# Kernel optimization log

Measured on AMD Instinct MI355X. Metric: run time of the kernel, lower is better.

The kernel has to match this reference:

```python
import jax, jax.numpy as jnp
import numpy as np
import math

IN_DIM = 2048
OUT_DIM = 2048
BATCH = 4096
BN_EPS = 1e-5


def setup_inputs() -> dict:
    key = jax.random.key(0)
    ks = jax.random.split(key, 6)
    x = jax.random.normal(ks[0], (BATCH, IN_DIM), dtype=jnp.float32)
    # scale ~ N(1.0, 0.1), translate = 0
    scale = 1.0 + 0.1 * jax.random.normal(ks[1], (1, IN_DIM), dtype=jnp.float32)
    translate = jnp.zeros((1, IN_DIM), dtype=jnp.float32)
    # kaiming-normal-ish init for wave_weight (fan_in), orthogonal-ish for base_weight
    wave_weight = jax.random.normal(ks[2], (OUT_DIM, IN_DIM), dtype=jnp.float32) * np.sqrt(2.0 / IN_DIM)
    bw = jax.random.normal(ks[3], (OUT_DIM, IN_DIM), dtype=jnp.float32)
    q, _ = jnp.linalg.qr(bw.T)  # (IN_DIM, OUT_DIM) orthonormal columns
    base_weight = q.T.astype(jnp.float32)
    gamma = jnp.ones((OUT_DIM,), dtype=jnp.float32)
    beta = jnp.zeros((OUT_DIM,), dtype=jnp.float32)
    return {"x": x, "scale": scale, "translate": translate,
            "wave_weight": wave_weight, "base_weight": base_weight,
            "gamma": gamma, "beta": beta}


def reference(x, scale, translate, wave_weight, base_weight, gamma, beta):
    # Bio wavelet: pi^-1/4 * cos(3u) * exp(-0.5 u^2), u = (x - t) / clamp(s, 1e-3)
    u = (x - translate) / jnp.maximum(scale, 1e-3)            # (B, in)
    wavelet = (math.pi ** -0.25) * jnp.cos(3.0 * u) * jnp.exp(-0.5 * u * u)
    # einsum 'boi,oi->bo' with singleton o broadcast == plain matmul
    wave_out = jnp.einsum('bi,oi->bo', wavelet, wave_weight)  # (B, out)
    base_out = jnp.einsum('bi,oi->bo', x, base_weight)        # (B, out)
    y = wave_out + 0.3 * base_out
    # BatchNorm1d (training mode: batch statistics, biased variance)
    mean = jnp.mean(y, axis=0)
    var = jnp.mean(jnp.square(y - mean), axis=0)
    out = gamma * (y - mean) * jax.lax.rsqrt(var + BN_EPS) + beta
    # dropout treated as identity (deterministic reference)
    return out
```

## Files before the change

kernel.cpp:

```cpp
#include <hip/hip_runtime.h>
#include <stdint.h>

#define IN_DIM 2048
#define OUT_DIM 2048
#define BATCH 4096
#define KDIM (2 * IN_DIM)
#define KROWB (KDIM * 2)
#define KH 2048
#define NTT 32
#define BN_EPS 1e-5f

typedef __attribute__((ext_vector_type(8))) short bf16x8;
typedef __attribute__((ext_vector_type(4))) float f32x4;

__device__ __forceinline__ unsigned short f2bf(float f) {
  union { float f; unsigned u; } v; v.f = f;
  unsigned r = v.u + 0x7FFFu + ((v.u >> 16) & 1u);
  return (unsigned short)(r >> 16);
}

__global__ void prep_act(const float* __restrict__ x,
                         const float* __restrict__ scale,
                         const float* __restrict__ translate,
                         unsigned short* __restrict__ A) {
  int e = (blockIdx.x * 256 + threadIdx.x) * 4;
  int b = e / IN_DIM;
  int i = e % IN_DIM;
  float4 xv = *(const float4*)(x + e);
  float4 sv = *(const float4*)(scale + i);
  float4 tv = *(const float4*)(translate + i);
  const float c = 0.7511255444649425f;
  float u0 = (xv.x - tv.x) / fmaxf(sv.x, 1e-3f);
  float u1 = (xv.y - tv.y) / fmaxf(sv.y, 1e-3f);
  float u2 = (xv.z - tv.z) / fmaxf(sv.z, 1e-3f);
  float u3 = (xv.w - tv.w) / fmaxf(sv.w, 1e-3f);
  ushort4 wv, xb;
  wv.x = f2bf(c * __cosf(3.0f * u0) * __expf(-0.5f * u0 * u0));
  wv.y = f2bf(c * __cosf(3.0f * u1) * __expf(-0.5f * u1 * u1));
  wv.z = f2bf(c * __cosf(3.0f * u2) * __expf(-0.5f * u2 * u2));
  wv.w = f2bf(c * __cosf(3.0f * u3) * __expf(-0.5f * u3 * u3));
  xb.x = f2bf(xv.x); xb.y = f2bf(xv.y); xb.z = f2bf(xv.z); xb.w = f2bf(xv.w);
  *(ushort4*)(A + (size_t)b * KDIM + i) = wv;
  *(ushort4*)(A + (size_t)b * KDIM + IN_DIM + i) = xb;
}

__global__ void prep_w(const float* __restrict__ ww,
                       const float* __restrict__ bw,
                       unsigned short* __restrict__ W) {
  int e = (blockIdx.x * 256 + threadIdx.x) * 4;
  int o = e / IN_DIM;
  int k = e % IN_DIM;
  float4 a = *(const float4*)(ww + e);
  float4 b = *(const float4*)(bw + e);
  ushort4 wa, wb;
  wa.x = f2bf(a.x); wa.y = f2bf(a.y); wa.z = f2bf(a.z); wa.w = f2bf(a.w);
  wb.x = f2bf(0.3f * b.x); wb.y = f2bf(0.3f * b.y);
  wb.z = f2bf(0.3f * b.z); wb.w = f2bf(0.3f * b.w);
  *(ushort4*)(W + (size_t)o * KDIM + k) = wa;
  *(ushort4*)(W + (size_t)o * KDIM + IN_DIM + k) = wb;
}


#define GLDS(gp, lo) __builtin_amdgcn_global_load_lds( \
    (const __attribute__((address_space(1))) void*)(gp), \
    (__attribute__((address_space(3))) void*)(lds + (lo) + ldsl), 16, 0, 0)

#define STG(u_, gp_, t_) do { \
  GLDS((gp_) + (size_t)(t_) * 128, (u_)); \
  GLDS((gp_) + (size_t)64 * KROWB + (size_t)(t_) * 128, (u_) + 8192); \
} while (0)

#define LDA4(mh, ss) do { \
  af[0] = *(const bf16x8*)(lds + P + rA + ((mh) * 4 + 0) * 2048 + (ss)); \
  af[1] = *(const bf16x8*)(lds + P + rA + ((mh) * 4 + 1) * 2048 + (ss)); \
  af[2] = *(const bf16x8*)(lds + P + rA + ((mh) * 4 + 2) * 2048 + (ss)); \
  af[3] = *(const bf16x8*)(lds + P + rA + ((mh) * 4 + 3) * 2048 + (ss)); \
} while (0)

#define LDB4(dst, ss) do { \
  dst[0] = *(const bf16x8*)(lds + P + rB + 0 * 2048 + (ss)); \
  dst[1] = *(const bf16x8*)(lds + P + rB + 1 * 2048 + (ss)); \
  dst[2] = *(const bf16x8*)(lds + P + rB + 2 * 2048 + (ss)); \
  dst[3] = *(const bf16x8*)(lds + P + rB + 3 * 2048 + (ss)); \
} while (0)

#define MM16(mh, bfr) do { \
  __builtin_amdgcn_s_setprio(1); \
  _Pragma("unroll") for (int i2 = 0; i2 < 4; ++i2) \
  _Pragma("unroll") for (int j2 = 0; j2 < 4; ++j2) \
    acc[(mh) * 4 + i2][j2] = __builtin_amdgcn_mfma_f32_16x16x32_bf16( \
        af[i2], bfr[j2], acc[(mh) * 4 + i2][j2], 0, 0, 0); \
  __builtin_amdgcn_s_setprio(0); \
} while (0)

#define LGKM0() asm volatile("s_waitcnt lgkmcnt(0)" ::: "memory")
#define VMW0()  asm volatile("s_waitcnt vmcnt(0)" ::: "memory")
#define BAR()   do { asm volatile("" ::: "memory"); __builtin_amdgcn_s_barrier(); \
                     asm volatile("" ::: "memory"); } while (0)

#define KTILE(u, DOST) do { \
  const int P = ((u) & 1) << 16; \
  const int Q = P ^ 65536; \
  LDA4(0, s0); LDB4(b0, s0); \
  if (DOST) { STG(Q + 32768, bS0, (u) + 1); STG(Q + 49152, bS1, (u) + 1); \
              STG(Q + 0, aS0, (u) + 1); STG(Q + 16384, aS1, (u) + 1); } \
  BAR(); MM16(0, b0); LGKM0(); BAR(); \
  LDA4(1, s0); \
  BAR(); MM16(1, b0); LGKM0(); BAR(); \
  LDA4(0, s1); LDB4(b1, s1); \
  BAR(); MM16(0, b1); LGKM0(); BAR(); \
  LDA4(1, s1); \
  BAR(); MM16(1, b1); LGKM0(); if (DOST) VMW0(); BAR(); \
} while (0)

__global__ __launch_bounds__(512, 2) void gemm256(
    const unsigned short* __restrict__ A,
    const unsigned short* __restrict__ W,
    float* __restrict__ P0, float* __restrict__ P1) {
  __shared__ char lds[131072];
  const int tid = threadIdx.x;
  const int lane = tid & 63;
  const int wave = tid >> 6;
  const int wm = wave >> 2;
  const int wn = wave & 3;

  const int sw = ((blockIdx.x & 7) << 5) | (blockIdx.x >> 3);
  const int kz = sw >> 7;
  const int brow = ((sw >> 3) & 15) * 256;
  const int bcol = (sw & 7) * 256;
  const size_t kb = (size_t)kz * (KH * 2);

  const int srow = tid >> 3;
  const int gc16 = (tid & 7) ^ (srow & 7);
  const char* aS0 = (const char*)A + (size_t)(brow + srow) * KROWB + kb + gc16 * 16;
  const char* aS1 = aS0 + (size_t)128 * KROWB;
  const char* bS0 = (const char*)W + (size_t)(bcol + srow) * KROWB + kb + gc16 * 16;
  const char* bS1 = bS0 + (size_t)128 * KROWB;
  const int ldsl = wave * 1024;

  const int rA = (wm * 128 + (lane & 15)) * 128;
  const int rB = 32768 + (wn * 64 + (lane & 15)) * 128;
  const int s0 = (((lane >> 4)    ) ^ (lane & 7)) << 4;
  const int s1 = ((4 + (lane >> 4)) ^ (lane & 7)) << 4;

  f32x4 acc[8][4];
#pragma unroll
  for (int m = 0; m < 8; ++m)
#pragma unroll
    for (int n = 0; n < 4; ++n)
      acc[m][n] = (f32x4){0.f, 0.f, 0.f, 0.f};
  bf16x8 af[4], b0[4], b1[4];

  STG(32768, bS0, 0); STG(49152, bS1, 0); STG(0, aS0, 0); STG(16384, aS1, 0);
  VMW0(); BAR();

  for (int u = 0; u < NTT - 1; ++u)
    KTILE(u, 1);
  KTILE(NTT - 1, 0);

  float* Pz = kz ? P1 : P0;
  const int r0 = brow + wm * 128 + (lane >> 4) * 4;
  const int c0 = bcol + wn * 64 + (lane & 15);
#pragma unroll
  for (int m = 0; m < 8; ++m)
#pragma unroll
    for (int n = 0; n < 4; ++n)
#pragma unroll
      for (int j = 0; j < 4; ++j)
        Pz[(size_t)(r0 + m * 16 + j) * OUT_DIM + (c0 + n * 16)] = acc[m][n][j];
}

__global__ void colstats2(const float* __restrict__ P0,
                          const float* __restrict__ P1,
                          float* __restrict__ sums, float* __restrict__ sqs) {
  int col = (blockIdx.x & 7) * 256 + threadIdx.x;
  int r0 = (blockIdx.x >> 3) * 128;
  float s = 0.f, q = 0.f;
  for (int r = 0; r < 128; ++r) {
    size_t idx = (size_t)(r0 + r) * OUT_DIM + col;
    float v = P0[idx] + P1[idx];
    s += v;
    q += v * v;
  }
  atomicAdd(&sums[col], s);
  atomicAdd(&sqs[col], q);
}

__global__ void bnorm2(const float* __restrict__ P1, float* __restrict__ Y,
                       const float* __restrict__ sums, const float* __restrict__ sqs,
                       const float* __restrict__ gamma, const float* __restrict__ beta) {
  int e = (blockIdx.x * 256 + threadIdx.x) * 4;
  int c = e % OUT_DIM;
  float4 y = *(float4*)(Y + e);
  float4 p = *(const float4*)(P1 + e);
  y.x += p.x; y.y += p.y; y.z += p.z; y.w += p.w;
  float4 s = *(const float4*)(sums + c);
  float4 q = *(const float4*)(sqs + c);
  float4 g = *(const float4*)(gamma + c);
  float4 bb = *(const float4*)(beta + c);
  const float invB = 1.0f / (float)BATCH;
  float m0 = s.x * invB, m1 = s.y * invB, m2 = s.z * invB, m3 = s.w * invB;
  float i0 = rsqrtf(q.x * invB - m0 * m0 + BN_EPS);
  float i1 = rsqrtf(q.y * invB - m1 * m1 + BN_EPS);
  float i2 = rsqrtf(q.z * invB - m2 * m2 + BN_EPS);
  float i3 = rsqrtf(q.w * invB - m3 * m3 + BN_EPS);
  y.x = g.x * (y.x - m0) * i0 + bb.x;
  y.y = g.y * (y.y - m1) * i1 + bb.y;
  y.z = g.z * (y.z - m2) * i2 + bb.z;
  y.w = g.w * (y.w - m3) * i3 + bb.w;
  *(float4*)(Y + e) = y;
}

extern "C" void kernel_launch(void* const* d_in, const int* in_sizes, int n_in,
                              void* d_out, int out_size, void* d_ws, size_t ws_size,
                              hipStream_t stream) {
  const float* x         = (const float*)d_in[0];
  const float* scale     = (const float*)d_in[1];
  const float* translate = (const float*)d_in[2];
  const float* ww        = (const float*)d_in[3];
  const float* bw        = (const float*)d_in[4];
  const float* gamma     = (const float*)d_in[5];
  const float* beta      = (const float*)d_in[6];
  float* out = (float*)d_out;

  char* ws = (char*)d_ws;
  unsigned short* A = (unsigned short*)ws;
  unsigned short* W = (unsigned short*)(ws + 33554432);
  float* P1   = (float*)(ws + 50331648);
  float* sums = (float*)(ws + 83886080);
  float* sqs  = sums + OUT_DIM;

  hipMemsetAsync(sums, 0, 2 * OUT_DIM * sizeof(float), stream);
  prep_act<<<(BATCH * IN_DIM) / 1024, 256, 0, stream>>>(x, scale, translate, A);
  prep_w<<<(OUT_DIM * IN_DIM) / 1024, 256, 0, stream>>>(ww, bw, W);
  gemm256<<<256, 512, 0, stream>>>(A, W, out, P1);
  colstats2<<<256, 256, 0, stream>>>(out, P1, sums, sqs);
  bnorm2<<<(BATCH * OUT_DIM) / 1024, 256, 0, stream>>>(P1, out, sums, sqs, gamma, beta);
}
```

Measured before the change: 125.3 us.

## Switch GEMM to four-stage LDS ring with 32-wide K tiles

```diff
diff --git a/kernel.cpp b/kernel.cpp
--- a/kernel.cpp
+++ b/kernel.cpp
@@ -7,7 +7,7 @@
 #define KDIM (2 * IN_DIM)
 #define KROWB (KDIM * 2)
 #define KH 2048
-#define NTT 32
+#define NTT 64
 #define BN_EPS 1e-5f
 
 typedef __attribute__((ext_vector_type(8))) short bf16x8;
@@ -65,25 +65,6 @@
     (const __attribute__((address_space(1))) void*)(gp), \
     (__attribute__((address_space(3))) void*)(lds + (lo) + ldsl), 16, 0, 0)
 
-#define STG(u_, gp_, t_) do { \
-  GLDS((gp_) + (size_t)(t_) * 128, (u_)); \
-  GLDS((gp_) + (size_t)64 * KROWB + (size_t)(t_) * 128, (u_) + 8192); \
-} while (0)
-
-#define LDA4(mh, ss) do { \
-  af[0] = *(const bf16x8*)(lds + P + rA + ((mh) * 4 + 0) * 2048 + (ss)); \
-  af[1] = *(const bf16x8*)(lds + P + rA + ((mh) * 4 + 1) * 2048 + (ss)); \
-  af[2] = *(const bf16x8*)(lds + P + rA + ((mh) * 4 + 2) * 2048 + (ss)); \
-  af[3] = *(const bf16x8*)(lds + P + rA + ((mh) * 4 + 3) * 2048 + (ss)); \
-} while (0)
-
-#define LDB4(dst, ss) do { \
-  dst[0] = *(const bf16x8*)(lds + P + rB + 0 * 2048 + (ss)); \
-  dst[1] = *(const bf16x8*)(lds + P + rB + 1 * 2048 + (ss)); \
-  dst[2] = *(const bf16x8*)(lds + P + rB + 2 * 2048 + (ss)); \
-  dst[3] = *(const bf16x8*)(lds + P + rB + 3 * 2048 + (ss)); \
-} while (0)
-
 #define MM16(mh, bfr) do { \
   __builtin_amdgcn_s_setprio(1); \
   _Pragma("unroll") for (int i2 = 0; i2 < 4; ++i2) \
@@ -94,23 +75,34 @@
 } while (0)
 
 #define LGKM0() asm volatile("s_waitcnt lgkmcnt(0)" ::: "memory")
+#define VMW8()  asm volatile("s_waitcnt vmcnt(8)" ::: "memory")
+#define VMW4()  asm volatile("s_waitcnt vmcnt(4)" ::: "memory")
 #define VMW0()  asm volatile("s_waitcnt vmcnt(0)" ::: "memory")
+#define NOW()   do { } while (0)
 #define BAR()   do { asm volatile("" ::: "memory"); __builtin_amdgcn_s_barrier(); \
                      asm volatile("" ::: "memory"); } while (0)
 
-#define KTILE(u, DOST) do { \
-  const int P = ((u) & 1) << 16; \
-  const int Q = P ^ 65536; \
-  LDA4(0, s0); LDB4(b0, s0); \
-  if (DOST) { STG(Q + 32768, bS0, (u) + 1); STG(Q + 49152, bS1, (u) + 1); \
-              STG(Q + 0, aS0, (u) + 1); STG(Q + 16384, aS1, (u) + 1); } \
-  BAR(); MM16(0, b0); LGKM0(); BAR(); \
-  LDA4(1, s0); \
-  BAR(); MM16(1, b0); LGKM0(); BAR(); \
-  LDA4(0, s1); LDB4(b1, s1); \
-  BAR(); MM16(0, b1); LGKM0(); BAR(); \
-  LDA4(1, s1); \
-  BAR(); MM16(1, b1); LGKM0(); if (DOST) VMW0(); BAR(); \
+#define KT(RS, SS, SOFS, DOST, TAILW) do { \
+  const char* Au = lds + ((RS) << 15) + wmOff; \
+  const char* Bu = lds + ((RS) << 15) + bnOff; \
+  af[0] = *(const bf16x8*)(Au + 0 * 1024 + roff); \
+  af[1] = *(const bf16x8*)(Au + 1 * 1024 + roff); \
+  af[2] = *(const bf16x8*)(Au + 2 * 1024 + roff); \
+  af[3] = *(const bf16x8*)(Au + 3 * 1024 + roff); \
+  bfr[0] = *(const bf16x8*)(Bu + 0 * 1024 + roff); \
+  bfr[1] = *(const bf16x8*)(Bu + 1 * 1024 + roff); \
+  bfr[2] = *(const bf16x8*)(Bu + 2 * 1024 + roff); \
+  bfr[3] = *(const bf16x8*)(Bu + 3 * 1024 + roff); \
+  if (DOST) { GLDS(a0p + (SOFS), ((SS) << 15) + 0); \
+              GLDS(a1p + (SOFS), ((SS) << 15) + 8192); } \
+  BAR(); MM16(0, bfr); LGKM0(); BAR(); \
+  af[0] = *(const bf16x8*)(Au + 4 * 1024 + roff); \
+  af[1] = *(const bf16x8*)(Au + 5 * 1024 + roff); \
+  af[2] = *(const bf16x8*)(Au + 6 * 1024 + roff); \
+  af[3] = *(const bf16x8*)(Au + 7 * 1024 + roff); \
+  if (DOST) { GLDS(b0p + (SOFS), ((SS) << 15) + 16384); \
+              GLDS(b1p + (SOFS), ((SS) << 15) + 24576); } \
+  BAR(); MM16(1, bfr); LGKM0(); TAILW; BAR(); \
 } while (0)
 
 __global__ __launch_bounds__(512, 2) void gemm256(
@@ -130,18 +122,19 @@
   const int bcol = (sw & 7) * 256;
   const size_t kb = (size_t)kz * (KH * 2);
 
-  const int srow = tid >> 3;
-  const int gc16 = (tid & 7) ^ (srow & 7);
-  const char* aS0 = (const char*)A + (size_t)(brow + srow) * KROWB + kb + gc16 * 16;
+  const int slr = tid >> 3;
+  const int srow2 = 2 * slr + ((tid >> 2) & 1);
+  const int skslot = (tid & 3) ^ (slr & 3);
+  const char* aS0 = (const char*)A + (size_t)(brow + srow2) * KROWB + kb + skslot * 16;
   const char* aS1 = aS0 + (size_t)128 * KROWB;
-  const char* bS0 = (const char*)W + (size_t)(bcol + srow) * KROWB + kb + gc16 * 16;
+  const char* bS0 = (const char*)W + (size_t)(bcol + srow2) * KROWB + kb + skslot * 16;
   const char* bS1 = bS0 + (size_t)128 * KROWB;
   const int ldsl = wave * 1024;
 
-  const int rA = (wm * 128 + (lane & 15)) * 128;
-  const int rB = 32768 + (wn * 64 + (lane & 15)) * 128;
-  const int s0 = (((lane >> 4)    ) ^ (lane & 7)) << 4;
-  const int s1 = ((4 + (lane >> 4)) ^ (lane & 7)) << 4;
+  const int lh = (lane & 15) >> 1;
+  const int roff = lh * 128 + (lane & 1) * 64 + (((lane >> 4) ^ (lh & 3)) << 4);
+  const int wmOff = wm * 8192;
+  const int bnOff = 16384 + (wn >> 1) * 8192 + (wn & 1) * 4096;
 
   f32x4 acc[8][4];
 #pragma unroll
@@ -149,14 +142,31 @@
 #pragma unroll
     for (int n = 0; n < 4; ++n)
       acc[m][n] = (f32x4){0.f, 0.f, 0.f, 0.f};
-  bf16x8 af[4], b0[4], b1[4];
-
-  STG(32768, bS0, 0); STG(49152, bS1, 0); STG(0, aS0, 0); STG(16384, aS1, 0);
-  VMW0(); BAR();
-
-  for (int u = 0; u < NTT - 1; ++u)
-    KTILE(u, 1);
-  KTILE(NTT - 1, 0);
+  bf16x8 af[4], bfr[4];
+
+  GLDS(aS0, 0); GLDS(aS1, 8192); GLDS(bS0, 16384); GLDS(bS1, 24576);
+  GLDS(aS0 + 64, 32768); GLDS(aS1 + 64, 32768 + 8192);
+  GLDS(bS0 + 64, 32768 + 16384); GLDS(bS1 + 64, 32768 + 24576);
+  GLDS(aS0 + 128, 65536); GLDS(aS1 + 128, 65536 + 8192);
+  GLDS(bS0 + 128, 65536 + 16384); GLDS(bS1 + 128, 65536 + 24576);
+  VMW8(); BAR();
+
+  const char* a0p = aS0 + 192;
+  const char* a1p = aS1 + 192;
+  const char* b0p = bS0 + 192;
+  const char* b1p = bS1 + 192;
+
+  for (int tt = 0; tt < 60; tt += 4) {
+    KT(0, 3, 0,   1, VMW8());
+    KT(1, 0, 64,  1, VMW8());
+    KT(2, 1, 128, 1, VMW8());
+    KT(3, 2, 192, 1, VMW8());
+    a0p += 256; a1p += 256; b0p += 256; b1p += 256;
+  }
+  KT(0, 3, 0, 1, VMW8());
+  KT(1, 0, 0, 0, VMW4());
+  KT(2, 0, 0, 0, VMW0());
+  KT(3, 0, 0, 0, NOW());
 
   float* Pz = kz ? P1 : P0;
   const int r0 = brow + wm * 128 + (lane >> 4) * 4;
```

After: 120.3 us. 1.04x faster.

## Deepen GEMM prefetch pipeline with split staging and vectorize column stats

Applied to the files above, without the earlier changes.

```diff
diff --git a/kernel.cpp b/kernel.cpp
--- a/kernel.cpp
+++ b/kernel.cpp
@@ -65,52 +65,60 @@
     (const __attribute__((address_space(1))) void*)(gp), \
     (__attribute__((address_space(3))) void*)(lds + (lo) + ldsl), 16, 0, 0)
 
-#define STG(u_, gp_, t_) do { \
-  GLDS((gp_) + (size_t)(t_) * 128, (u_)); \
-  GLDS((gp_) + (size_t)64 * KROWB + (size_t)(t_) * 128, (u_) + 8192); \
-} while (0)
-
-#define LDA4(mh, ss) do { \
-  af[0] = *(const bf16x8*)(lds + P + rA + ((mh) * 4 + 0) * 2048 + (ss)); \
-  af[1] = *(const bf16x8*)(lds + P + rA + ((mh) * 4 + 1) * 2048 + (ss)); \
-  af[2] = *(const bf16x8*)(lds + P + rA + ((mh) * 4 + 2) * 2048 + (ss)); \
-  af[3] = *(const bf16x8*)(lds + P + rA + ((mh) * 4 + 3) * 2048 + (ss)); \
-} while (0)
-
-#define LDB4(dst, ss) do { \
-  dst[0] = *(const bf16x8*)(lds + P + rB + 0 * 2048 + (ss)); \
-  dst[1] = *(const bf16x8*)(lds + P + rB + 1 * 2048 + (ss)); \
-  dst[2] = *(const bf16x8*)(lds + P + rB + 2 * 2048 + (ss)); \
-  dst[3] = *(const bf16x8*)(lds + P + rB + 3 * 2048 + (ss)); \
-} while (0)
-
-#define MM16(mh, bfr) do { \
+#define STG2(gp_, lo_) do { \
+  GLDS((gp_), (lo_)); \
+  GLDS((gp_) + (size_t)64 * KROWB, (lo_) + 8192); \
+} while (0)
+
+#define LDA(mh, ro) do { \
+  af[0] = *(const bf16x8*)(lds + P + AuO + (mh) * 8192 + 0 * 2048 + (ro)); \
+  af[1] = *(const bf16x8*)(lds + P + AuO + (mh) * 8192 + 1 * 2048 + (ro)); \
+  af[2] = *(const bf16x8*)(lds + P + AuO + (mh) * 8192 + 2 * 2048 + (ro)); \
+  af[3] = *(const bf16x8*)(lds + P + AuO + (mh) * 8192 + 3 * 2048 + (ro)); \
+} while (0)
+
+#define LDB(dst, ro) do { \
+  dst[0] = *(const bf16x8*)(lds + P + BuO + 0 * 2048 + (ro)); \
+  dst[1] = *(const bf16x8*)(lds + P + BuO + 1 * 2048 + (ro)); \
+  dst[2] = *(const bf16x8*)(lds + P + BuO + 2 * 2048 + (ro)); \
+  dst[3] = *(const bf16x8*)(lds + P + BuO + 3 * 2048 + (ro)); \
+} while (0)
+
+#define MM16(mh, bq) do { \
   __builtin_amdgcn_s_setprio(1); \
   _Pragma("unroll") for (int i2 = 0; i2 < 4; ++i2) \
   _Pragma("unroll") for (int j2 = 0; j2 < 4; ++j2) \
     acc[(mh) * 4 + i2][j2] = __builtin_amdgcn_mfma_f32_16x16x32_bf16( \
-        af[i2], bfr[j2], acc[(mh) * 4 + i2][j2], 0, 0, 0); \
+        af[i2], bq[j2], acc[(mh) * 4 + i2][j2], 0, 0, 0); \
   __builtin_amdgcn_s_setprio(0); \
 } while (0)
 
 #define LGKM0() asm volatile("s_waitcnt lgkmcnt(0)" ::: "memory")
+#define VMW6()  asm volatile("s_waitcnt vmcnt(6)" ::: "memory")
 #define VMW0()  asm volatile("s_waitcnt vmcnt(0)" ::: "memory")
+#define NOW()   do { } while (0)
 #define BAR()   do { asm volatile("" ::: "memory"); __builtin_amdgcn_s_barrier(); \
                      asm volatile("" ::: "memory"); } while (0)
 
-#define KTILE(u, DOST) do { \
-  const int P = ((u) & 1) << 16; \
+#define KTILE(m, DO1, DO4, TAILW) do { \
+  const int P = ((m) & 1) << 16; \
   const int Q = P ^ 65536; \
-  LDA4(0, s0); LDB4(b0, s0); \
-  if (DOST) { STG(Q + 32768, bS0, (u) + 1); STG(Q + 49152, bS1, (u) + 1); \
-              STG(Q + 0, aS0, (u) + 1); STG(Q + 16384, aS1, (u) + 1); } \
-  BAR(); MM16(0, b0); LGKM0(); BAR(); \
-  LDA4(1, s0); \
-  BAR(); MM16(1, b0); LGKM0(); BAR(); \
-  LDA4(0, s1); LDB4(b1, s1); \
-  BAR(); MM16(0, b1); LGKM0(); BAR(); \
-  LDA4(1, s1); \
-  BAR(); MM16(1, b1); LGKM0(); if (DOST) VMW0(); BAR(); \
+   \
+  LDA(0, ro0); LDB(b0, ro0); \
+  if (DO1) STG2(aP1 + (size_t)((m) + 1) * 128, Q + 16384); \
+  BAR(); LGKM0(); MM16(0, b0); BAR(); \
+   \
+  LDA(1, ro0); \
+  BAR(); LGKM0(); MM16(1, b0); BAR(); \
+   \
+  LDA(0, ro1); LDB(b1, ro1); \
+  BAR(); LGKM0(); MM16(0, b1); BAR(); \
+   \
+  LDA(1, ro1); \
+  if (DO4) { STG2(aP0 + (size_t)((m) + 2) * 128, P); \
+             STG2(bP0 + (size_t)((m) + 2) * 128, P + 32768); \
+             STG2(bP1 + (size_t)((m) + 2) * 128, P + 49152); } \
+  BAR(); LGKM0(); MM16(1, b1); TAILW; BAR(); \
 } while (0)
 
 __global__ __launch_bounds__(512, 2) void gemm256(
@@ -131,17 +139,17 @@
   const size_t kb = (size_t)kz * (KH * 2);
 
   const int srow = tid >> 3;
-  const int gc16 = (tid & 7) ^ (srow & 7);
-  const char* aS0 = (const char*)A + (size_t)(brow + srow) * KROWB + kb + gc16 * 16;
-  const char* aS1 = aS0 + (size_t)128 * KROWB;
-  const char* bS0 = (const char*)W + (size_t)(bcol + srow) * KROWB + kb + gc16 * 16;
-  const char* bS1 = bS0 + (size_t)128 * KROWB;
+  const int skslot = (tid & 7) ^ (srow & 7);
+  const char* aP0 = (const char*)A + (size_t)(brow + srow) * KROWB + kb + skslot * 16;
+  const char* aP1 = aP0 + (size_t)128 * KROWB;
+  const char* bP0 = (const char*)W + (size_t)(bcol + srow) * KROWB + kb + skslot * 16;
+  const char* bP1 = bP0 + (size_t)128 * KROWB;
   const int ldsl = wave * 1024;
 
-  const int rA = (wm * 128 + (lane & 15)) * 128;
-  const int rB = 32768 + (wn * 64 + (lane & 15)) * 128;
-  const int s0 = (((lane >> 4)    ) ^ (lane & 7)) << 4;
-  const int s1 = ((4 + (lane >> 4)) ^ (lane & 7)) << 4;
+  const int ro0 = (lane & 15) * 128 + ((((lane >> 4)    ) ^ (lane & 7)) << 4);
+  const int ro1 = (lane & 15) * 128 + ((((lane >> 4) + 4) ^ (lane & 7)) << 4);
+  const int AuO = wm * 16384;
+  const int BuO = 32768 + (wn >> 1) * 16384 + (wn & 1) * 8192;
 
   f32x4 acc[8][4];
 #pragma unroll
@@ -151,12 +159,16 @@
       acc[m][n] = (f32x4){0.f, 0.f, 0.f, 0.f};
   bf16x8 af[4], b0[4], b1[4];
 
-  STG(32768, bS0, 0); STG(49152, bS1, 0); STG(0, aS0, 0); STG(16384, aS1, 0);
-  VMW0(); BAR();
-
-  for (int u = 0; u < NTT - 1; ++u)
-    KTILE(u, 1);
-  KTILE(NTT - 1, 0);
+  STG2(aP0, 0); STG2(aP1, 16384); STG2(bP0, 32768); STG2(bP1, 49152);
+  STG2(aP0 + 128, 65536);
+  STG2(bP0 + 128, 65536 + 32768);
+  STG2(bP1 + 128, 65536 + 49152);
+  VMW6(); BAR();
+
+  for (int m = 0; m < NTT - 2; ++m)
+    KTILE(m, 1, 1, VMW6());
+  KTILE(NTT - 2, 1, 0, VMW0());
+  KTILE(NTT - 1, 0, 0, NOW());
 
   float* Pz = kz ? P1 : P0;
   const int r0 = brow + wm * 128 + (lane >> 4) * 4;
@@ -173,17 +185,21 @@
 __global__ void colstats2(const float* __restrict__ P0,
                           const float* __restrict__ P1,
                           float* __restrict__ sums, float* __restrict__ sqs) {
-  int col = (blockIdx.x & 7) * 256 + threadIdx.x;
-  int r0 = (blockIdx.x >> 3) * 128;
-  float s = 0.f, q = 0.f;
-  for (int r = 0; r < 128; ++r) {
-    size_t idx = (size_t)(r0 + r) * OUT_DIM + col;
-    float v = P0[idx] + P1[idx];
-    s += v;
-    q += v * v;
+  int c4 = (blockIdx.x & 1) * 256 + threadIdx.x;
+  int r0 = (blockIdx.x >> 1) * 32;
+  float4 s = {0.f, 0.f, 0.f, 0.f}, q = {0.f, 0.f, 0.f, 0.f};
+  for (int r = 0; r < 32; ++r) {
+    size_t idx = (size_t)(r0 + r) * (OUT_DIM / 4) + c4;
+    float4 a = ((const float4*)P0)[idx];
+    float4 b = ((const float4*)P1)[idx];
+    float v0 = a.x + b.x, v1 = a.y + b.y, v2 = a.z + b.z, v3 = a.w + b.w;
+    s.x += v0; s.y += v1; s.z += v2; s.w += v3;
+    q.x += v0 * v0; q.y += v1 * v1; q.z += v2 * v2; q.w += v3 * v3;
   }
-  atomicAdd(&sums[col], s);
-  atomicAdd(&sqs[col], q);
+  atomicAdd(&sums[c4 * 4 + 0], s.x); atomicAdd(&sums[c4 * 4 + 1], s.y);
+  atomicAdd(&sums[c4 * 4 + 2], s.z); atomicAdd(&sums[c4 * 4 + 3], s.w);
+  atomicAdd(&sqs[c4 * 4 + 0], q.x); atomicAdd(&sqs[c4 * 4 + 1], q.y);
+  atomicAdd(&sqs[c4 * 4 + 2], q.z); atomicAdd(&sqs[c4 * 4 + 3], q.w);
 }
 
 __global__ void bnorm2(const float* __restrict__ P1, float* __restrict__ Y,
```

Measured after the change: 133.0 us. 6.2% more time.
